# Kernel optimization log

Hardware: AMD Instinct MI355X
Metric: run time of the kernel (lower is better)

## Reference

```python
import jax, jax.numpy as jnp
import numpy as np


def setup_inputs() -> dict:
    key = jax.random.key(0)
    C, S, NQ, H = 10, 10, 30, 1024  # n_classes, n_support, n_query, h_dim
    ks = jax.random.split(key, 6)
    x = jax.random.normal(ks[0], (C * (S + NQ), H), dtype=jnp.float32)
    # sorted, balanced labels so y.eq(c).nonzero() picks contiguous blocks
    y = jnp.repeat(jnp.arange(C, dtype=jnp.int32), S + NQ)
    W1 = jax.random.normal(ks[1], (H, H), dtype=jnp.float32) / np.sqrt(H)
    b1 = jnp.zeros((H,), dtype=jnp.float32)
    W2 = jax.random.normal(ks[2], (4 * H, H), dtype=jnp.float32) / np.sqrt(4 * H)
    b2 = jnp.zeros((H,), dtype=jnp.float32)
    return {"x": x, "W1": W1, "b1": b1, "W2": W2, "b2": b2,
            "y": y, "n_classes": C, "n_support": S, "n_query": NQ, "flag": 0}


def reference(x, W1, b1, W2, b2, y, n_classes, n_support, n_query, flag):
    # flag == 0 path; y is sorted & balanced, so the label-based gather in the
    # original (y.eq(c).nonzero()[:S] / [S:]) reduces to a reshape.
    C, S, NQ = n_classes, n_support, n_query
    H = x.shape[-1]
    xr = x.reshape(C, S + NQ, H)
    support = xr[:, :S]                      # [C, S, H]
    query = xr[:, S:].reshape(C * NQ, H)     # [Qt, H], Qt = C*NQ

    # fc1 computed ONCE on support/query, then broadcast (same math as
    # applying fc1 to the expanded tensors in the original).
    sf = jnp.einsum('csh,hd->csd', support, W1) + b1   # [C, S, H]
    qf = query @ W1 + b1                               # [Qt, H]

    # fc2 on concat([sf, qf, |sf-qf|, sf*qf]) split into 4 blocks of W2 so we
    # never materialize the [Qt, C, S, 4H] concat.
    Ws, Wq, Wc, Wd = W2[:H], W2[H:2 * H], W2[2 * H:3 * H], W2[3 * H:]
    a_s = jnp.einsum('csh,hd->csd', sf, Ws)            # [C, S, H]
    a_q = qf @ Wq                                      # [Qt, H]
    sfb = sf[None]                                     # [1, C, S, H]
    qfb = qf[:, None, None]                            # [Qt, 1, 1, H]
    d1 = jnp.abs(sfb - qfb)                            # [Qt, C, S, H]
    d2 = sfb * qfb                                     # [Qt, C, S, H]
    mca_ = (a_s[None] + a_q[:, None, None]
            + jnp.einsum('qcsh,hd->qcsd', d1, Wc)
            + jnp.einsum('qcsh,hd->qcsd', d2, Wd) + b2)  # [Qt, C, S, H]

    score = jax.nn.softmax(jnp.tanh(mca_).sum(-1), axis=-1)  # [Qt, C, S]
    proto = jnp.einsum('qcs,csh->qch', score, support)       # [Qt, C, H]
    dists = jnp.sum((proto - query[:, None, :]) ** 2, axis=-1)  # [Qt, C]
    return dists
```

## Files before the change

### kernel.cpp

```cpp
#include <hip/hip_runtime.h>
#include <hip/hip_bf16.h>
#include <math.h>

#define C_   10
#define S_   10
#define NQ_  30
#define H_   1024
#define Q_   300
#define ROWS_ 400

typedef __attribute__((ext_vector_type(8))) short s16x8;
typedef __attribute__((ext_vector_type(4))) float f32x4;

static __device__ __forceinline__ short f2b(float f) {
  __hip_bfloat16 h = __float2bfloat16(f);
  return __builtin_bit_cast(short, h);
}

static __device__ __forceinline__ float ftanh(float v) {
  v = fminf(fmaxf(v, -10.f), 10.f);
  float e = __expf(2.f * v);
  return (e - 1.f) / (e + 1.f);
}

__global__ __launch_bounds__(256) void feat_kernel(
    const float* __restrict__ x, const float* __restrict__ W1,
    const float* __restrict__ b1, float* __restrict__ f) {
  __shared__ float xs[4][H_];
  const int rt = blockIdx.x % 100;
  const int nt = blockIdx.x / 100;
  const int r0 = rt * 4;
  const int n0 = nt * 256;
  const int tid = threadIdx.x;

  for (int t = tid; t < 4 * H_ / 4; t += 256) {
    int r = t >> 8, h4 = (t & 255) * 4;
    *(float4*)&xs[r][h4] = *(const float4*)&x[(size_t)(r0 + r) * H_ + h4];
  }
  __syncthreads();

  float acc0 = 0.f, acc1 = 0.f, acc2 = 0.f, acc3 = 0.f;
  const float* __restrict__ wp = W1 + n0 + tid;
#pragma unroll 8
  for (int h = 0; h < H_; ++h) {
    float w = wp[(size_t)h * H_];
    acc0 = fmaf(xs[0][h], w, acc0);
    acc1 = fmaf(xs[1][h], w, acc1);
    acc2 = fmaf(xs[2][h], w, acc2);
    acc3 = fmaf(xs[3][h], w, acc3);
  }
  const int col = n0 + tid;
  const float bb = b1[col];
  f[(size_t)(r0 + 0) * H_ + col] = acc0 + bb;
  f[(size_t)(r0 + 1) * H_ + col] = acc1 + bb;
  f[(size_t)(r0 + 2) * H_ + col] = acc2 + bb;
  f[(size_t)(r0 + 3) * H_ + col] = acc3 + bb;
}

__global__ __launch_bounds__(256) void proj_kernel(
    const float* __restrict__ f, const float* __restrict__ W2,
    const float* __restrict__ b2, float* __restrict__ a) {
  __shared__ float fs[4][H_];
  const int rt = blockIdx.x % 100;
  const int nt = blockIdx.x / 100;
  const bool isSup = (rt < 25);
  const int i0 = isSup ? rt * 4 : (rt - 25) * 4;
  const int n0 = nt * 256;
  const float* __restrict__ W = isSup ? W2 : (W2 + (size_t)H_ * H_);
  const int tid = threadIdx.x;

  for (int t = tid; t < 4 * H_ / 4; t += 256) {
    int r = t >> 8, h4 = (t & 255) * 4;
    int i = i0 + r;
    int row = isSup ? ((i / 10) * 40 + (i % 10)) : ((i / 30) * 40 + 10 + (i % 30));
    *(float4*)&fs[r][h4] = *(const float4*)&f[(size_t)row * H_ + h4];
  }
  __syncthreads();

  float acc0 = 0.f, acc1 = 0.f, acc2 = 0.f, acc3 = 0.f;
  const float* __restrict__ wp = W + n0 + tid;
#pragma unroll 8
  for (int h = 0; h < H_; ++h) {
    float w = wp[(size_t)h * H_];
    acc0 = fmaf(fs[0][h], w, acc0);
    acc1 = fmaf(fs[1][h], w, acc1);
    acc2 = fmaf(fs[2][h], w, acc2);
    acc3 = fmaf(fs[3][h], w, acc3);
  }
  const int col = n0 + tid;
  const float bb = isSup ? 0.f : b2[col];
  const int o0 = isSup ? i0 : (100 + i0);
  a[(size_t)(o0 + 0) * H_ + col] = acc0 + bb;
  a[(size_t)(o0 + 1) * H_ + col] = acc1 + bb;
  a[(size_t)(o0 + 2) * H_ + col] = acc2 + bb;
  a[(size_t)(o0 + 3) * H_ + col] = acc3 + bb;
}

__global__ __launch_bounds__(256) void trans_kernel(
    const float* __restrict__ W2, unsigned short* __restrict__ Bt,
    float* __restrict__ logits) {
  const int b = blockIdx.x;
  const int tid = threadIdx.x;
  if (b == 512) {
    float4* lz = (float4*)logits;
    for (int i = tid; i < 7500; i += 256) lz[i] = make_float4(0.f, 0.f, 0.f, 0.f);
    return;
  }
  const int mat = b >> 8, kt = (b >> 4) & 15, ntl = b & 15;
  const float* __restrict__ src =
      W2 + (size_t)(2 + mat) * H_ * H_ + (size_t)(kt * 64) * H_ + ntl * 64;
  __shared__ float tl[64][65];
  {
    int r = tid >> 2, c4 = (tid & 3) * 16;
    const float* srcp = src + (size_t)r * H_ + c4;
#pragma unroll
    for (int j = 0; j < 4; ++j) {
      float4 v = *(const float4*)(srcp + j * 4);
      tl[r][c4 + j * 4 + 0] = v.x;
      tl[r][c4 + j * 4 + 1] = v.y;
      tl[r][c4 + j * 4 + 2] = v.z;
      tl[r][c4 + j * 4 + 3] = v.w;
    }
  }
  __syncthreads();
  {
    int n = tid >> 2, k0t = (tid & 3) * 16;
    s16x8 o0, o1;
#pragma unroll
    for (int j = 0; j < 8; ++j) {
      o0[j] = f2b(tl[k0t + j][n]);
      o1[j] = f2b(tl[k0t + 8 + j][n]);
    }
    unsigned short* dstp = Bt + (size_t)mat * H_ * H_ +
                           (size_t)(ntl * 64 + n) * H_ + kt * 64 + k0t;
    *(s16x8*)dstp = o0;
    *(s16x8*)(dstp + 8) = o1;
  }
}

__global__ __launch_bounds__(512, 2) void mca_mfma_kernel(
    const float* __restrict__ f, const float* __restrict__ a,
    const unsigned short* __restrict__ Bt, float* __restrict__ logits) {
  const int b = blockIdx.x;
  const int nt = b & 3;
  const int qt = (b >> 2) % 19;
  const int c = (b >> 2) / 19;
  const int q0 = qt * 16;
  const int n0 = nt * 256;

  __shared__ unsigned short Als[2][160 * 64];
  __shared__ unsigned short Bls[2][256 * 64];

  const int tid = threadIdx.x;
  const int w = tid >> 6, lane = tid & 63;

  const int row0 = tid >> 2, qtr = tid & 3;
  const int qloc0 = row0 / 10, s0 = row0 - qloc0 * 10;
  int q0g = q0 + qloc0; if (q0g > 299) q0g = 299;
  const float* sfp0 = f + (size_t)(c * 40 + s0) * H_ + qtr * 8;
  const float* qfp0 = f + (size_t)((q0g / 30) * 40 + 10 + (q0g % 30)) * H_ + qtr * 8;
  const unsigned asw0 = (unsigned)((row0 & 7) << 4);
  const unsigned aw0 = (unsigned)(row0 * 128 + qtr * 16);
  const bool has2 = (tid < 128);
  const int row1 = row0 + 128;
  const int qloc1 = row1 / 10, s1 = row1 - qloc1 * 10;
  int q1g = q0 + qloc1; if (q1g > 299) q1g = 299;
  const float* sfp1 = f + (size_t)(c * 40 + s1) * H_ + qtr * 8;
  const float* qfp1 = f + (size_t)((q1g / 30) * 40 + 10 + (q1g % 30)) * H_ + qtr * 8;
  const unsigned asw1 = (unsigned)((row1 & 7) << 4);
  const unsigned aw1 = (unsigned)(row1 * 128 + qtr * 16);

  const int bn = tid >> 1, bm = tid & 1;
  const unsigned short* bp = Bt + (size_t)bm * H_ * H_ + (size_t)(n0 + bn) * H_;
  const unsigned bw = (unsigned)(bn * 128 + bm * 64);
  const unsigned bsw = (unsigned)((bn & 7) << 4);

  const int frow = lane & 15;
  const unsigned fkb = (unsigned)((lane >> 4) * 16);
  const unsigned swf = (unsigned)((frow & 7) << 4);
  const int wr = w >> 2, wc = w & 3;
  unsigned ard[5], brd[4];
#pragma unroll
  for (int m = 0; m < 5; ++m) ard[m] = (unsigned)((wr * 80 + m * 16 + frow) * 128);
#pragma unroll
  for (int nf = 0; nf < 4; ++nf) brd[nf] = (unsigned)((wc * 64 + nf * 16 + frow) * 128);

  f32x4 acc[5][4];
#pragma unroll
  for (int m = 0; m < 5; ++m)
#pragma unroll
    for (int nf = 0; nf < 4; ++nf) acc[m][nf] = (f32x4)(0.f);

  float4 SA0, SB0, QA0, QB0, SA1, SB1, QA1, QB1;
  s16x8 B0, B1, B2, B3;

#define ISSUE(KG)                                                              \
  do {                                                                         \
    SA0 = *(const float4*)(sfp0 + (KG));                                       \
    SB0 = *(const float4*)(sfp0 + (KG) + 4);                                   \
    QA0 = *(const float4*)(qfp0 + (KG));                                       \
    QB0 = *(const float4*)(qfp0 + (KG) + 4);                                   \
    if (has2) {                                                                \
      SA1 = *(const float4*)(sfp1 + (KG));                                     \
      SB1 = *(const float4*)(sfp1 + (KG) + 4);                                 \
      QA1 = *(const float4*)(qfp1 + (KG));                                     \
      QB1 = *(const float4*)(qfp1 + (KG) + 4);                                 \
    }                                                                          \
    B0 = *(const s16x8*)(bp + (KG));                                           \
    B1 = *(const s16x8*)(bp + (KG) + 8);                                       \
    B2 = *(const s16x8*)(bp + (KG) + 16);                                      \
    B3 = *(const s16x8*)(bp + (KG) + 24);                                      \
  } while (0)

#define GEN1(SA, SB, QA, QB, AWR, ASW, AB)                                     \
  do {                                                                         \
    s16x8 d1, d2;                                                              \
    d1[0] = f2b(fabsf(SA.x - QA.x)); d2[0] = f2b(SA.x * QA.x);                 \
    d1[1] = f2b(fabsf(SA.y - QA.y)); d2[1] = f2b(SA.y * QA.y);                 \
    d1[2] = f2b(fabsf(SA.z - QA.z)); d2[2] = f2b(SA.z * QA.z);                 \
    d1[3] = f2b(fabsf(SA.w - QA.w)); d2[3] = f2b(SA.w * QA.w);                 \
    d1[4] = f2b(fabsf(SB.x - QB.x)); d2[4] = f2b(SB.x * QB.x);                 \
    d1[5] = f2b(fabsf(SB.y - QB.y)); d2[5] = f2b(SB.y * QB.y);                 \
    d1[6] = f2b(fabsf(SB.z - QB.z)); d2[6] = f2b(SB.z * QB.z);                 \
    d1[7] = f2b(fabsf(SB.w - QB.w)); d2[7] = f2b(SB.w * QB.w);                 \
    *(s16x8*)((AB) + ((AWR) ^ (ASW))) = d1;                                    \
    *(s16x8*)((AB) + (((AWR) + 64) ^ (ASW))) = d2;                             \
  } while (0)

#define WTILE(P)                                                               \
  do {                                                                         \
    char* AB = (char*)&Als[P][0];                                              \
    char* BB = (char*)&Bls[P][0];                                              \
    *(s16x8*)(BB + ((bw + 0) ^ bsw)) = B0;                                     \
    *(s16x8*)(BB + ((bw + 16) ^ bsw)) = B1;                                    \
    *(s16x8*)(BB + ((bw + 32) ^ bsw)) = B2;                                    \
    *(s16x8*)(BB + ((bw + 48) ^ bsw)) = B3;                                    \
    GEN1(SA0, SB0, QA0, QB0, aw0, asw0, AB);                                   \
    if (has2) GEN1(SA1, SB1, QA1, QB1, aw1, asw1, AB);                         \
  } while (0)

#define MFMA_PHASE(P)                                                          \
  do {                                                                         \
    const char* AB = (const char*)&Als[P][0];                                  \
    const char* BB = (const char*)&Bls[P][0];                                  \
    _Pragma("unroll") for (int kk = 0; kk < 2; ++kk) {                         \
      const unsigned kb = fkb + kk * 64;                                       \
      s16x8 bf0 = *(const s16x8*)(BB + ((brd[0] + kb) ^ swf));                 \
      s16x8 bf1 = *(const s16x8*)(BB + ((brd[1] + kb) ^ swf));                 \
      s16x8 bf2 = *(const s16x8*)(BB + ((brd[2] + kb) ^ swf));                 \
      s16x8 bf3 = *(const s16x8*)(BB + ((brd[3] + kb) ^ swf));                 \
      _Pragma("unroll") for (int m = 0; m < 5; ++m) {                          \
        s16x8 af = *(const s16x8*)(AB + ((ard[m] + kb) ^ swf));                \
        acc[m][0] = __builtin_amdgcn_mfma_f32_16x16x32_bf16(af, bf0, acc[m][0], 0, 0, 0); \
        acc[m][1] = __builtin_amdgcn_mfma_f32_16x16x32_bf16(af, bf1, acc[m][1], 0, 0, 0); \
        acc[m][2] = __builtin_amdgcn_mfma_f32_16x16x32_bf16(af, bf2, acc[m][2], 0, 0, 0); \
        acc[m][3] = __builtin_amdgcn_mfma_f32_16x16x32_bf16(af, bf3, acc[m][3], 0, 0, 0); \
      }                                                                        \
    }                                                                          \
  } while (0)

  ISSUE(0);
  WTILE(0);
  __syncthreads();

  int p = 0;
  for (int ks = 0; ks < 32; ++ks) {
    const int kn = (ks < 31 ? ks + 1 : 31) * 32;
    ISSUE(kn);
    __builtin_amdgcn_s_setprio(1);
    MFMA_PHASE(p);
    __builtin_amdgcn_s_setprio(0);
    if (ks < 31) WTILE(p ^ 1);
    __syncthreads();
    p ^= 1;
  }

  const int colb = n0 + wc * 64 + frow;
  const int rgrp = (lane >> 4) * 4;
#pragma unroll
  for (int m = 0; m < 5; ++m) {
#pragma unroll
    for (int r = 0; r < 4; ++r) {
      const int row = wr * 80 + m * 16 + rgrp + r;
      const int qloc = row / 10, s = row - qloc * 10;
      const int q = q0 + qloc;
      float t = 0.f;
#pragma unroll
      for (int nf = 0; nf < 4; ++nf) {
        const int col = colb + nf * 16;
        float v = acc[m][nf][r] + a[(size_t)(c * 10 + s) * H_ + col] +
                  a[(size_t)(100 + q) * H_ + col];
        t += ftanh(v);
      }
      t += __shfl_xor(t, 1);
      t += __shfl_xor(t, 2);
      t += __shfl_xor(t, 4);
      t += __shfl_xor(t, 8);
      if ((lane & 15) == 0 && q < 300)
        atomicAdd(&logits[(q * 10 + c) * 10 + s], t);
    }
  }
#undef ISSUE
#undef GEN1
#undef WTILE
#undef MFMA_PHASE
}

__global__ __launch_bounds__(256) void out_kernel(
    const float* __restrict__ x, const float* __restrict__ logits,
    float* __restrict__ dists) {
  const int q = blockIdx.x / 10;
  const int c = blockIdx.x % 10;
  const int tid = threadIdx.x;
  const int lane = tid & 63;
  const int wave = tid >> 6;
  __shared__ float red[4];

  float l[S_];
  float m = -1e30f;
#pragma unroll
  for (int s = 0; s < S_; ++s) {
    l[s] = logits[(q * 10 + c) * 10 + s];
    m = fmaxf(m, l[s]);
  }
  float sum = 0.f;
  float sc[S_];
#pragma unroll
  for (int s = 0; s < S_; ++s) {
    sc[s] = __expf(l[s] - m);
    sum += sc[s];
  }
  float inv = 1.f / sum;
#pragma unroll
  for (int s = 0; s < S_; ++s) sc[s] *= inv;

  const int qr = (q / 30) * 40 + 10 + (q % 30);
  float part = 0.f;
#pragma unroll
  for (int ii = 0; ii < 4; ++ii) {
    int i = tid + ii * 256;
    float p = 0.f;
#pragma unroll
    for (int s = 0; s < S_; ++s)
      p = fmaf(sc[s], x[(size_t)(c * 40 + s) * H_ + i], p);
    float d = p - x[(size_t)qr * H_ + i];
    part = fmaf(d, d, part);
  }
  for (int off = 32; off; off >>= 1) part += __shfl_down(part, off);
  if (lane == 0) red[wave] = part;
  __syncthreads();
  if (tid == 0) dists[q * 10 + c] = red[0] + red[1] + red[2] + red[3];
}

extern "C" void kernel_launch(void* const* d_in, const int* in_sizes, int n_in,
                              void* d_out, int out_size, void* d_ws, size_t ws_size,
                              hipStream_t stream) {
  const float* x = (const float*)d_in[0];
  const float* W1 = (const float*)d_in[1];
  const float* b1 = (const float*)d_in[2];
  const float* W2 = (const float*)d_in[3];
  const float* b2 = (const float*)d_in[4];
  float* out = (float*)d_out;

  float* f = (float*)d_ws;
  float* a = f + ROWS_ * H_;
  float* logits = a + ROWS_ * H_;
  unsigned short* Bt = (unsigned short*)(logits + 30208);

  feat_kernel<<<400, 256, 0, stream>>>(x, W1, b1, f);
  proj_kernel<<<400, 256, 0, stream>>>(f, W2, b2, a);
  trans_kernel<<<513, 256, 0, stream>>>(W2, Bt, logits);
  mca_mfma_kernel<<<10 * 19 * 4, 512, 0, stream>>>(f, a, Bt, logits);
  out_kernel<<<3000, 256, 0, stream>>>(x, logits, out);
}
```

Measured before the change: 325.4 us.

## Halve MCA block N-tile and load B tiles via direct global-to-LDS DMA

The MFMA kernel now uses 256-thread blocks covering 128 output columns instead of 512 threads covering 256, doubling the grid to 1520 blocks. The A-tile generation is redistributed so each thread builds up to three rows. B-tile loading switches from register loads plus swizzled LDS stores to global_load_lds DMA, with the XOR swizzle folded into the source addresses. The intent is to cut the VGPR and VALU cost of staging B and to improve occupancy and load balance. In exchange, each block regenerates the elementwise A tile for fewer output columns, so that work is duplicated across twice as many blocks.

```diff
diff --git a/kernel.cpp b/kernel.cpp
--- a/kernel.cpp
+++ b/kernel.cpp
@@ -138,47 +138,55 @@
   }
 }
 
-__global__ __launch_bounds__(512, 2) void mca_mfma_kernel(
+__global__ __launch_bounds__(256, 2) void mca_mfma_kernel(
     const float* __restrict__ f, const float* __restrict__ a,
     const unsigned short* __restrict__ Bt, float* __restrict__ logits) {
   const int b = blockIdx.x;
-  const int nt = b & 3;
-  const int qt = (b >> 2) % 19;
-  const int c = (b >> 2) / 19;
+  const int nt = b & 7;
+  const int qt = (b >> 3) % 19;
+  const int c = (b >> 3) / 19;
   const int q0 = qt * 16;
-  const int n0 = nt * 256;
+  const int n0 = nt * 128;
 
   __shared__ unsigned short Als[2][160 * 64];
-  __shared__ unsigned short Bls[2][256 * 64];
+  __shared__ unsigned short Bls[2][128 * 64];
 
   const int tid = threadIdx.x;
   const int w = tid >> 6, lane = tid & 63;
 
-  const int row0 = tid >> 2, qtr = tid & 3;
-  const int qloc0 = row0 / 10, s0 = row0 - qloc0 * 10;
-  int q0g = q0 + qloc0; if (q0g > 299) q0g = 299;
-  const float* sfp0 = f + (size_t)(c * 40 + s0) * H_ + qtr * 8;
-  const float* qfp0 = f + (size_t)((q0g / 30) * 40 + 10 + (q0g % 30)) * H_ + qtr * 8;
-  const unsigned asw0 = (unsigned)((row0 & 7) << 4);
-  const unsigned aw0 = (unsigned)(row0 * 128 + qtr * 16);
+  const int rbase = tid >> 2, qtr = tid & 3;
   const bool has2 = (tid < 128);
-  const int row1 = row0 + 128;
-  const int qloc1 = row1 / 10, s1 = row1 - qloc1 * 10;
-  int q1g = q0 + qloc1; if (q1g > 299) q1g = 299;
-  const float* sfp1 = f + (size_t)(c * 40 + s1) * H_ + qtr * 8;
-  const float* qfp1 = f + (size_t)((q1g / 30) * 40 + 10 + (q1g % 30)) * H_ + qtr * 8;
-  const unsigned asw1 = (unsigned)((row1 & 7) << 4);
-  const unsigned aw1 = (unsigned)(row1 * 128 + qtr * 16);
-
-  const int bn = tid >> 1, bm = tid & 1;
-  const unsigned short* bp = Bt + (size_t)bm * H_ * H_ + (size_t)(n0 + bn) * H_;
-  const unsigned bw = (unsigned)(bn * 128 + bm * 64);
-  const unsigned bsw = (unsigned)((bn & 7) << 4);
+  const float* sfp[3];
+  const float* qfp[3];
+  unsigned awv[3], aswv[3];
+#pragma unroll
+  for (int j = 0; j < 3; ++j) {
+    int row = (j < 2) ? (rbase + j * 64) : (128 + rbase);
+    int qloc = row / 10, s = row - qloc * 10;
+    int qg = q0 + qloc;
+    if (qg > 299) qg = 299;
+    sfp[j] = f + (size_t)(c * 40 + s) * H_ + qtr * 8;
+    qfp[j] = f + (size_t)((qg / 30) * 40 + 10 + (qg % 30)) * H_ + qtr * 8;
+    aswv[j] = (unsigned)((row & 7) << 4);
+    awv[j] = (unsigned)(row * 128 + qtr * 16);
+  }
+
+  const int rlo = lane >> 3;
+  const int cch = (lane & 7) ^ rlo;
+  const unsigned short* bsrc[4];
+  unsigned bldso[4];
+#pragma unroll
+  for (int i = 0; i < 4; ++i) {
+    int row = w * 32 + i * 8 + rlo;
+    bsrc[i] = Bt + (size_t)(cch >> 2) * H_ * H_ + (size_t)(n0 + row) * H_ +
+              (cch & 3) * 8;
+    bldso[i] = (unsigned)(w * 4096 + i * 1024);
+  }
 
   const int frow = lane & 15;
   const unsigned fkb = (unsigned)((lane >> 4) * 16);
   const unsigned swf = (unsigned)((frow & 7) << 4);
-  const int wr = w >> 2, wc = w & 3;
+  const int wr = w >> 1, wc = w & 1;
   unsigned ard[5], brd[4];
 #pragma unroll
   for (int m = 0; m < 5; ++m) ard[m] = (unsigned)((wr * 80 + m * 16 + frow) * 128);
@@ -191,52 +199,55 @@
 #pragma unroll
     for (int nf = 0; nf < 4; ++nf) acc[m][nf] = (f32x4)(0.f);
 
-  float4 SA0, SB0, QA0, QB0, SA1, SB1, QA1, QB1;
-  s16x8 B0, B1, B2, B3;
+  float4 SA[3], SB[3], QA[3], QB[3];
+
+#define DMA_B(P, KG)                                                           \
+  do {                                                                         \
+    _Pragma("unroll") for (int i = 0; i < 4; ++i) {                            \
+      __builtin_amdgcn_global_load_lds(                                        \
+          (const __attribute__((address_space(1))) unsigned int*)(bsrc[i] + (KG)), \
+          (__attribute__((address_space(3))) unsigned int*)((char*)&Bls[P][0] + bldso[i]), \
+          16, 0, 0);                                                           \
+    }                                                                          \
+  } while (0)
 
 #define ISSUE(KG)                                                              \
   do {                                                                         \
-    SA0 = *(const float4*)(sfp0 + (KG));                                       \
-    SB0 = *(const float4*)(sfp0 + (KG) + 4);                                   \
-    QA0 = *(const float4*)(qfp0 + (KG));                                       \
-    QB0 = *(const float4*)(qfp0 + (KG) + 4);                                   \
+    _Pragma("unroll") for (int j = 0; j < 2; ++j) {                            \
+      SA[j] = *(const float4*)(sfp[j] + (KG));                                 \
+      SB[j] = *(const float4*)(sfp[j] + (KG) + 4);                             \
+      QA[j] = *(const float4*)(qfp[j] + (KG));                                 \
+      QB[j] = *(const float4*)(qfp[j] + (KG) + 4);                             \
+    }                                                                          \
     if (has2) {                                                                \
-      SA1 = *(const float4*)(sfp1 + (KG));                                     \
-      SB1 = *(const float4*)(sfp1 + (KG) + 4);                                 \
-      QA1 = *(const float4*)(qfp1 + (KG));                                     \
-      QB1 = *(const float4*)(qfp1 + (KG) + 4);                                 \
+      SA[2] = *(const float4*)(sfp[2] + (KG));                                 \
+      SB[2] = *(const float4*)(sfp[2] + (KG) + 4);                             \
+      QA[2] = *(const float4*)(qfp[2] + (KG));                                 \
+      QB[2] = *(const float4*)(qfp[2] + (KG) + 4);                             \
     }                                                                          \
-    B0 = *(const s16x8*)(bp + (KG));                                           \
-    B1 = *(const s16x8*)(bp + (KG) + 8);                                       \
-    B2 = *(const s16x8*)(bp + (KG) + 16);                                      \
-    B3 = *(const s16x8*)(bp + (KG) + 24);                                      \
-  } while (0)
-
-#define GEN1(SA, SB, QA, QB, AWR, ASW, AB)                                     \
+  } while (0)
+
+#define GEN1(J, AB)                                                            \
   do {                                                                         \
     s16x8 d1, d2;                                                              \
-    d1[0] = f2b(fabsf(SA.x - QA.x)); d2[0] = f2b(SA.x * QA.x);                 \
-    d1[1] = f2b(fabsf(SA.y - QA.y)); d2[1] = f2b(SA.y * QA.y);                 \
-    d1[2] = f2b(fabsf(SA.z - QA.z)); d2[2] = f2b(SA.z * QA.z);                 \
-    d1[3] = f2b(fabsf(SA.w - QA.w)); d2[3] = f2b(SA.w * QA.w);                 \
-    d1[4] = f2b(fabsf(SB.x - QB.x)); d2[4] = f2b(SB.x * QB.x);                 \
-    d1[5] = f2b(fabsf(SB.y - QB.y)); d2[5] = f2b(SB.y * QB.y);                 \
-    d1[6] = f2b(fabsf(SB.z - QB.z)); d2[6] = f2b(SB.z * QB.z);                 \
-    d1[7] = f2b(fabsf(SB.w - QB.w)); d2[7] = f2b(SB.w * QB.w);                 \
-    *(s16x8*)((AB) + ((AWR) ^ (ASW))) = d1;                                    \
-    *(s16x8*)((AB) + (((AWR) + 64) ^ (ASW))) = d2;                             \
+    d1[0] = f2b(fabsf(SA[J].x - QA[J].x)); d2[0] = f2b(SA[J].x * QA[J].x);     \
+    d1[1] = f2b(fabsf(SA[J].y - QA[J].y)); d2[1] = f2b(SA[J].y * QA[J].y);     \
+    d1[2] = f2b(fabsf(SA[J].z - QA[J].z)); d2[2] = f2b(SA[J].z * QA[J].z);     \
+    d1[3] = f2b(fabsf(SA[J].w - QA[J].w)); d2[3] = f2b(SA[J].w * QA[J].w);     \
+    d1[4] = f2b(fabsf(SB[J].x - QB[J].x)); d2[4] = f2b(SB[J].x * QB[J].x);     \
+    d1[5] = f2b(fabsf(SB[J].y - QB[J].y)); d2[5] = f2b(SB[J].y * QB[J].y);     \
+    d1[6] = f2b(fabsf(SB[J].z - QB[J].z)); d2[6] = f2b(SB[J].z * QB[J].z);     \
+    d1[7] = f2b(fabsf(SB[J].w - QB[J].w)); d2[7] = f2b(SB[J].w * QB[J].w);     \
+    *(s16x8*)((AB) + (awv[J] ^ aswv[J])) = d1;                                 \
+    *(s16x8*)((AB) + ((awv[J] + 64) ^ aswv[J])) = d2;                          \
   } while (0)
 
 #define WTILE(P)                                                               \
   do {                                                                         \
     char* AB = (char*)&Als[P][0];                                              \
-    char* BB = (char*)&Bls[P][0];                                              \
-    *(s16x8*)(BB + ((bw + 0) ^ bsw)) = B0;                                     \
-    *(s16x8*)(BB + ((bw + 16) ^ bsw)) = B1;                                    \
-    *(s16x8*)(BB + ((bw + 32) ^ bsw)) = B2;                                    \
-    *(s16x8*)(BB + ((bw + 48) ^ bsw)) = B3;                                    \
-    GEN1(SA0, SB0, QA0, QB0, aw0, asw0, AB);                                   \
-    if (has2) GEN1(SA1, SB1, QA1, QB1, aw1, asw1, AB);                         \
+    GEN1(0, AB);                                                               \
+    GEN1(1, AB);                                                               \
+    if (has2) GEN1(2, AB);                                                     \
   } while (0)
 
 #define MFMA_PHASE(P)                                                          \
@@ -259,14 +270,17 @@
     }                                                                          \
   } while (0)
 
+  DMA_B(0, 0);
   ISSUE(0);
   WTILE(0);
   __syncthreads();
 
   int p = 0;
   for (int ks = 0; ks < 32; ++ks) {
-    const int kn = (ks < 31 ? ks + 1 : 31) * 32;
-    ISSUE(kn);
+    if (ks < 31) {
+      DMA_B(p ^ 1, (ks + 1) * 32);
+      ISSUE((ks + 1) * 32);
+    }
     __builtin_amdgcn_s_setprio(1);
     MFMA_PHASE(p);
     __builtin_amdgcn_s_setprio(0);
@@ -300,6 +314,7 @@
         atomicAdd(&logits[(q * 10 + c) * 10 + s], t);
     }
   }
+#undef DMA_B
 #undef ISSUE
 #undef GEN1
 #undef WTILE
@@ -370,6 +385,6 @@
   feat_kernel<<<400, 256, 0, stream>>>(x, W1, b1, f);
   proj_kernel<<<400, 256, 0, stream>>>(f, W2, b2, a);
   trans_kernel<<<513, 256, 0, stream>>>(W2, Bt, logits);
-  mca_mfma_kernel<<<10 * 19 * 4, 512, 0, stream>>>(f, a, Bt, logits);
+  mca_mfma_kernel<<<10 * 19 * 8, 256, 0, stream>>>(f, a, Bt, logits);
   out_kernel<<<3000, 256, 0, stream>>>(x, logits, out);
 }
```

Measured after the change: 330.2 us. About the same (+1.5%).
